# Kernel optimization log

Measured on AMD Instinct MI355X. Metric: run time of the kernel, lower is better.

Reference implementation:

```python
import jax, jax.numpy as jnp
import numpy as np

B, S, D = 4, 2048, 1024
H, HD = 16, 64  # num_heads, head_dim = qkv_features // num_heads


def setup_inputs() -> dict:
  key = jax.random.key(0)
  ks = jax.random.split(key, 11)
  s = 0.02
  return {
    'inputs_q': jax.random.normal(ks[0], (B, S, D), jnp.float32),
    'inputs_k': jax.random.normal(ks[1], (B, S, D), jnp.float32),
    'inputs_v': jax.random.normal(ks[2], (B, S, D), jnp.float32),
    # LinearGeneral kernels: [in_features, num_heads, head_dim]
    'Wq': jax.random.normal(ks[3], (D, H, HD), jnp.float32) * s,
    'bq': jnp.zeros((H, HD), jnp.float32),
    'Wk': jax.random.normal(ks[4], (D, H, HD), jnp.float32) * s,
    'bk': jnp.zeros((H, HD), jnp.float32),
    'Wv': jax.random.normal(ks[5], (D, H, HD), jnp.float32) * s,
    'bv': jnp.zeros((H, HD), jnp.float32),
    # output LinearGeneral kernel: [num_heads, head_dim, out_features]
    'Wo': jax.random.normal(ks[6], (H, HD, D), jnp.float32) * s,
    'bo': jnp.zeros((D,), jnp.float32),
  }


def reference(inputs_q, inputs_k, inputs_v, Wq, bq, Wk, bk, Wv, bv, Wo, bo):
  # q/k/v projections -> [B, S, H, HD]
  q = jnp.einsum('bsf,fhd->bshd', inputs_q, Wq) + bq
  k = jnp.einsum('bsf,fhd->bshd', inputs_k, Wk) + bk
  v = jnp.einsum('bsf,fhd->bshd', inputs_v, Wv) + bv
  # scaled dot-product attention (naive full softmax, as in the module)
  depth = q.shape[-1]
  q = q / jnp.sqrt(jnp.asarray(depth, q.dtype))
  attn = jnp.einsum('bqhd,bkhd->bhqk', q, k)  # [B, H, S, S]
  attn = jax.nn.softmax(attn, axis=-1)
  x = jnp.einsum('bhqk,bkhd->bqhd', attn, v)  # [B, S, H, HD]
  # output projection -> [B, S, D]
  out = jnp.einsum('bqhd,hdo->bqo', x, Wo) + bo
  return out
```

## Files before the change

kernel.cpp:

```cpp
#include <hip/hip_runtime.h>


typedef __attribute__((ext_vector_type(4))) float f32x4;
typedef __attribute__((ext_vector_type(8))) short short8;
typedef unsigned short u16;
typedef unsigned int u32;

__device__ __forceinline__ u16 f2bf(float f) {
  u32 u = __builtin_bit_cast(u32, f);
  u += 0x7fffu + ((u >> 16) & 1u);
  return (u16)(u >> 16);
}

__device__ __forceinline__ void gload16(const u16* g, u16* l) {
  __builtin_amdgcn_global_load_lds((const __attribute__((address_space(1))) void*)g,
                                   (__attribute__((address_space(3))) void*)l, 16, 0, 0);
}

__global__ __launch_bounds__(256) void cvt_f32_bf16(const float* __restrict__ in,
                                                    u16* __restrict__ out) {
  int i = blockIdx.x * 256 + threadIdx.x;
  float4 v = ((const float4*)in)[i];
  ushort4 o;
  o.x = f2bf(v.x); o.y = f2bf(v.y); o.z = f2bf(v.z); o.w = f2bf(v.w);
  ((ushort4*)out)[i] = o;
}

__global__ __launch_bounds__(256) void transpose_w(const float* __restrict__ src,
                                                   u16* __restrict__ dst) {
  __shared__ float t[64][65];
  const int bx = blockIdx.x * 64;
  const int by = blockIdx.y * 64;
  const int tid = threadIdx.x;
  const int c4 = (tid & 15) * 4, r = tid >> 4;
#pragma unroll
  for (int i = 0; i < 4; ++i) {
    int row = r + i * 16;
    float4 v = *(const float4*)&src[(size_t)(by + row) * 1024 + bx + c4];
    t[row][c4] = v.x; t[row][c4 + 1] = v.y; t[row][c4 + 2] = v.z; t[row][c4 + 3] = v.w;
  }
  __syncthreads();
#pragma unroll
  for (int i = 0; i < 4; ++i) {
    int nrow = r + i * 16;
    ushort4 o;
    o.x = f2bf(t[c4 + 0][nrow]); o.y = f2bf(t[c4 + 1][nrow]);
    o.z = f2bf(t[c4 + 2][nrow]); o.w = f2bf(t[c4 + 3][nrow]);
    *(ushort4*)&dst[(size_t)(bx + nrow) * 1024 + by + c4] = o;
  }
}

template <int EPI>
__global__ __launch_bounds__(256) void gemm_k1024(const u16* __restrict__ A,
                                                  const u16* __restrict__ Bt,
                                                  const float* __restrict__ bias,
                                                  void* __restrict__ outp) {
  __shared__ u16 lds[2 * 8192];
  u16* ldsA = lds;
  u16* ldsB = lds + 8192;
  const int tid = threadIdx.x, ln = tid & 63, wv = tid >> 6;
  const int wr = wv >> 1, wc = wv & 1;
  const int lq = ln & 15, g = ln >> 4;
  const int m0 = blockIdx.y * 128, n0 = blockIdx.x * 128;
  f32x4 acc[4][4] = {};

  for (int kt = 0; kt < 16; ++kt) {
    const int k0 = kt * 64;
#pragma unroll
    for (int c = 0; c < 4; ++c) {
      int chunk = c * 256 + wv * 64 + ln;
      int row = chunk >> 3, cc = chunk & 7;
      gload16(A + (size_t)(m0 + row) * 1024 + k0 + ((cc ^ (row & 7)) << 3),
              ldsA + (c * 256 + wv * 64) * 8);
    }
#pragma unroll
    for (int c = 0; c < 4; ++c) {
      int chunk = c * 256 + wv * 64 + ln;
      int row = chunk >> 3, cc = chunk & 7;
      gload16(Bt + (size_t)(n0 + row) * 1024 + k0 + ((cc ^ (row & 7)) << 3),
              ldsB + (c * 256 + wv * 64) * 8);
    }
    __syncthreads();
#pragma unroll
    for (int ks = 0; ks < 2; ++ks) {
      short8 af[4], bf[4];
#pragma unroll
      for (int m = 0; m < 4; ++m) {
        int rA = wr * 64 + m * 16 + lq;
        int cc = (ks * 4 + g) ^ (rA & 7);
        af[m] = *(const short8*)&ldsA[rA * 64 + cc * 8];
      }
#pragma unroll
      for (int n = 0; n < 4; ++n) {
        int rB = wc * 64 + n * 16 + lq;
        int cc = (ks * 4 + g) ^ (rB & 7);
        bf[n] = *(const short8*)&ldsB[rB * 64 + cc * 8];
      }
#pragma unroll
      for (int m = 0; m < 4; ++m)
#pragma unroll
        for (int n = 0; n < 4; ++n)
          acc[m][n] = __builtin_amdgcn_mfma_f32_16x16x32_bf16(af[m], bf[n], acc[m][n], 0, 0, 0);
    }
    __syncthreads();
  }

#pragma unroll
  for (int m = 0; m < 4; ++m) {
#pragma unroll
    for (int n = 0; n < 4; ++n) {
      const int row = m0 + wr * 64 + m * 16 + g * 4;
      const int col = n0 + wc * 64 + n * 16 + lq;
      const float bb = bias[col];
      if constexpr (EPI == 0 || EPI == 1) {
        u16* O = (u16*)outp;
        int b = row >> 11, s = row & 2047, h = col >> 6, d = col & 63;
        size_t base = ((size_t)(b * 16 + h) * 2048 + s) * 64 + d;
#pragma unroll
        for (int j = 0; j < 4; ++j) {
          float v = acc[m][n][j] + bb;
          if constexpr (EPI == 0) v *= 0.18033688f;
          O[base + (size_t)j * 64] = f2bf(v);
        }
      } else if constexpr (EPI == 2) {
        u16* O = (u16*)outp;
        int b = row >> 11, s = row & 2047, h = col >> 6, d = col & 63;
        ushort4 pk;
        pk.x = f2bf(acc[m][n][0] + bb); pk.y = f2bf(acc[m][n][1] + bb);
        pk.z = f2bf(acc[m][n][2] + bb); pk.w = f2bf(acc[m][n][3] + bb);
        *(ushort4*)&O[((size_t)(b * 16 + h) * 64 + d) * 2048 + s] = pk;
      } else {
        float* O = (float*)outp;
#pragma unroll
        for (int j = 0; j < 4; ++j) O[(size_t)(row + j) * 1024 + col] = acc[m][n][j] + bb;
      }
    }
  }
}

__global__ __launch_bounds__(256) void attn_kernel(const u16* __restrict__ Q,
                                                   const u16* __restrict__ K,
                                                   const u16* __restrict__ Vt,
                                                   u16* __restrict__ Xat) {
  __shared__ u16 lds[4096 + 4096 + 4 * 32 * 72];
  u16* ldsK = lds;
  u16* ldsV = lds + 4096;
  const int tid = threadIdx.x, ln = tid & 63, wv = tid >> 6;
  const int lq = ln & 15, g = ln >> 4;
  const int bh = blockIdx.y;
  const int q0 = blockIdx.x * 128 + wv * 32;
  u16* myP = lds + 8192 + wv * 32 * 72;

  const u16* Qb = Q + ((size_t)bh * 2048 + q0) * 64;
  const u16* Kb = K + (size_t)bh * 2048 * 64;
  const u16* Vb = Vt + (size_t)bh * 64 * 2048;

  short8 qf[2][2];
#pragma unroll
  for (int qb = 0; qb < 2; ++qb)
#pragma unroll
    for (int ks = 0; ks < 2; ++ks)
      qf[qb][ks] = *(const short8*)&Qb[(size_t)(qb * 16 + lq) * 64 + ks * 32 + g * 8];

  f32x4 accO[2][4] = {};
  float lsum[2] = {0.f, 0.f};

  for (int kv = 0; kv < 32; ++kv) {
    const int s0 = kv * 64;
#pragma unroll
    for (int c = 0; c < 2; ++c) {
      int chunk = c * 256 + wv * 64 + ln;
      int row = chunk >> 3, cc = chunk & 7;
      gload16(Kb + (size_t)(s0 + row) * 64 + ((cc ^ (row & 7)) << 3),
              ldsK + (c * 256 + wv * 64) * 8);
    }
#pragma unroll
    for (int c = 0; c < 2; ++c) {
      int chunk = c * 256 + wv * 64 + ln;
      int row = chunk >> 3, cc = chunk & 7;
      gload16(Vb + (size_t)row * 2048 + s0 + ((cc ^ (row & 7)) << 3),
              ldsV + (c * 256 + wv * 64) * 8);
    }
    __syncthreads();

    f32x4 accS[4][2] = {};
#pragma unroll
    for (int ks = 0; ks < 2; ++ks) {
      short8 kf[4];
#pragma unroll
      for (int m = 0; m < 4; ++m) {
        int r = m * 16 + lq;
        int cc = (ks * 4 + g) ^ (r & 7);
        kf[m] = *(const short8*)&ldsK[r * 64 + cc * 8];
      }
#pragma unroll
      for (int m = 0; m < 4; ++m)
#pragma unroll
        for (int qb = 0; qb < 2; ++qb)
          accS[m][qb] = __builtin_amdgcn_mfma_f32_16x16x32_bf16(kf[m], qf[qb][ks], accS[m][qb], 0, 0, 0);
    }

#pragma unroll
    for (int qb = 0; qb < 2; ++qb) {
      float p[16];
#pragma unroll
      for (int m = 0; m < 4; ++m)
#pragma unroll
        for (int j = 0; j < 4; ++j) {
          float v = exp2f(accS[m][qb][j]);
          p[m * 4 + j] = v;
          lsum[qb] += v;
        }
#pragma unroll
      for (int m = 0; m < 4; ++m) {
        u32 w0, w1;
        asm("v_cvt_pk_bf16_f32 %0, %1, %2" : "=v"(w0) : "v"(p[m * 4 + 0]), "v"(p[m * 4 + 1]));
        asm("v_cvt_pk_bf16_f32 %0, %1, %2" : "=v"(w1) : "v"(p[m * 4 + 2]), "v"(p[m * 4 + 3]));
        uint2 w; w.x = w0; w.y = w1;
        *(uint2*)&myP[(qb * 16 + lq) * 72 + m * 16 + g * 4] = w;
      }
    }

#pragma unroll
    for (int ks = 0; ks < 2; ++ks) {
      short8 pf[2];
#pragma unroll
      for (int qb = 0; qb < 2; ++qb)
        pf[qb] = *(const short8*)&myP[(qb * 16 + lq) * 72 + ks * 32 + g * 8];
#pragma unroll
      for (int n = 0; n < 4; ++n) {
        int r = n * 16 + lq;
        int cc = (ks * 4 + g) ^ (r & 7);
        short8 vf = *(const short8*)&ldsV[r * 64 + cc * 8];
#pragma unroll
        for (int qb = 0; qb < 2; ++qb)
          accO[qb][n] = __builtin_amdgcn_mfma_f32_16x16x32_bf16(pf[qb], vf, accO[qb][n], 0, 0, 0);
      }
    }
    __syncthreads();
  }

  const int b = bh >> 4, h = bh & 15;
#pragma unroll
  for (int qb = 0; qb < 2; ++qb) {
    float t = lsum[qb];
    t += __shfl_xor(t, 16);
    t += __shfl_xor(t, 32);
    float inv = 1.0f / t;
    float inv_row[4];
#pragma unroll
    for (int j = 0; j < 4; ++j) inv_row[j] = __shfl(inv, g * 4 + j);
#pragma unroll
    for (int n = 0; n < 4; ++n)
#pragma unroll
      for (int j = 0; j < 4; ++j) {
        int s = q0 + qb * 16 + g * 4 + j;
        Xat[((size_t)b * 2048 + s) * 1024 + h * 64 + n * 16 + lq] = f2bf(accO[qb][n][j] * inv_row[j]);
      }
  }
}

extern "C" void kernel_launch(void* const* d_in, const int* in_sizes, int n_in,
                              void* d_out, int out_size, void* d_ws, size_t ws_size,
                              hipStream_t stream) {
  const float* xq = (const float*)d_in[0];
  const float* xk = (const float*)d_in[1];
  const float* xv = (const float*)d_in[2];
  const float* Wq = (const float*)d_in[3];
  const float* bq = (const float*)d_in[4];
  const float* Wk = (const float*)d_in[5];
  const float* bk = (const float*)d_in[6];
  const float* Wv = (const float*)d_in[7];
  const float* bv = (const float*)d_in[8];
  const float* Wo = (const float*)d_in[9];
  const float* bo = (const float*)d_in[10];

  char* ws = (char*)d_ws;
  u16* Xqb = (u16*)(ws + 0);
  u16* Xkb = (u16*)(ws + 16777216);
  u16* Xvb = (u16*)(ws + 33554432);
  u16* Wtq = (u16*)(ws + 50331648);
  u16* Wtk = (u16*)(ws + 52428800);
  u16* Wtv = (u16*)(ws + 54525952);
  u16* Wot = (u16*)(ws + 56623104);
  u16* Qb  = (u16*)(ws + 58720256);
  u16* Kb  = (u16*)(ws + 75497472);
  u16* Vtb = (u16*)(ws + 92274688);
  u16* Xat = Xqb;

  cvt_f32_bf16<<<8192, 256, 0, stream>>>(xq, Xqb);
  cvt_f32_bf16<<<8192, 256, 0, stream>>>(xk, Xkb);
  cvt_f32_bf16<<<8192, 256, 0, stream>>>(xv, Xvb);

  transpose_w<<<dim3(16, 16), 256, 0, stream>>>(Wq, Wtq);
  transpose_w<<<dim3(16, 16), 256, 0, stream>>>(Wk, Wtk);
  transpose_w<<<dim3(16, 16), 256, 0, stream>>>(Wv, Wtv);
  transpose_w<<<dim3(16, 16), 256, 0, stream>>>(Wo, Wot);

  gemm_k1024<0><<<dim3(8, 64), 256, 0, stream>>>(Xqb, Wtq, bq, Qb);
  gemm_k1024<1><<<dim3(8, 64), 256, 0, stream>>>(Xkb, Wtk, bk, Kb);
  gemm_k1024<2><<<dim3(8, 64), 256, 0, stream>>>(Xvb, Wtv, bv, Vtb);

  attn_kernel<<<dim3(16, 64), 256, 0, stream>>>(Qb, Kb, Vtb, Xat);

  gemm_k1024<3><<<dim3(8, 64), 256, 0, stream>>>(Xat, Wot, bo, d_out);
}
```

Measured before the change: 394.5 us.

## Double-buffer attention K/V loads, compute row sums via MFMA, batch prep kernels

The attention kernel now double-buffers K/V tiles in LDS, issuing the next tile's async global-to-LDS loads before computing the current one, so memory latency overlaps with the MFMA work. Softmax row sums are now accumulated with an extra MFMA against a ones vector instead of scalar adds and cross-lane shuffles. The three f32-to-bf16 conversions and four weight transposes are each merged into a single launch. The changes cost twice the K/V LDS, which may reduce occupancy, plus extra barriers, and the row sums are now taken from bf16-rounded probabilities.

```diff
diff --git a/kernel.cpp b/kernel.cpp
--- a/kernel.cpp
+++ b/kernel.cpp
@@ -17,8 +17,14 @@
                                    (__attribute__((address_space(3))) void*)l, 16, 0, 0);
 }
 
-__global__ __launch_bounds__(256) void cvt_f32_bf16(const float* __restrict__ in,
-                                                    u16* __restrict__ out) {
+__global__ __launch_bounds__(256) void cvt_f32_bf16_3(const float* __restrict__ a,
+                                                      const float* __restrict__ b,
+                                                      const float* __restrict__ c,
+                                                      u16* __restrict__ oa,
+                                                      u16* __restrict__ ob,
+                                                      u16* __restrict__ oc) {
+  const float* in = blockIdx.y == 0 ? a : (blockIdx.y == 1 ? b : c);
+  u16* out = blockIdx.y == 0 ? oa : (blockIdx.y == 1 ? ob : oc);
   int i = blockIdx.x * 256 + threadIdx.x;
   float4 v = ((const float4*)in)[i];
   ushort4 o;
@@ -26,8 +32,16 @@
   ((ushort4*)out)[i] = o;
 }
 
-__global__ __launch_bounds__(256) void transpose_w(const float* __restrict__ src,
-                                                   u16* __restrict__ dst) {
+__global__ __launch_bounds__(256) void transpose_w4(const float* __restrict__ s0,
+                                                    const float* __restrict__ s1,
+                                                    const float* __restrict__ s2,
+                                                    const float* __restrict__ s3,
+                                                    u16* __restrict__ d0,
+                                                    u16* __restrict__ d1,
+                                                    u16* __restrict__ d2,
+                                                    u16* __restrict__ d3) {
+  const float* src = blockIdx.z == 0 ? s0 : (blockIdx.z == 1 ? s1 : (blockIdx.z == 2 ? s2 : s3));
+  u16* dst = blockIdx.z == 0 ? d0 : (blockIdx.z == 1 ? d1 : (blockIdx.z == 2 ? d2 : d3));
   __shared__ float t[64][65];
   const int bx = blockIdx.x * 64;
   const int by = blockIdx.y * 64;
@@ -142,14 +156,16 @@
                                                    const u16* __restrict__ K,
                                                    const u16* __restrict__ Vt,
                                                    u16* __restrict__ Xat) {
-  __shared__ u16 lds[4096 + 4096 + 4 * 32 * 72];
-  u16* ldsK = lds;
-  u16* ldsV = lds + 4096;
+  __shared__ u16 lds[4 * 4096 + 4 * 32 * 72];
+  u16* ldsK0 = lds;
+  u16* ldsK1 = lds + 4096;
+  u16* ldsV0 = lds + 8192;
+  u16* ldsV1 = lds + 12288;
   const int tid = threadIdx.x, ln = tid & 63, wv = tid >> 6;
   const int lq = ln & 15, g = ln >> 4;
   const int bh = blockIdx.y;
   const int q0 = blockIdx.x * 128 + wv * 32;
-  u16* myP = lds + 8192 + wv * 32 * 72;
+  u16* myP = lds + 16384 + wv * 32 * 72;
 
   const u16* Qb = Q + ((size_t)bh * 2048 + q0) * 64;
   const u16* Kb = K + (size_t)bh * 2048 * 64;
@@ -162,27 +178,31 @@
     for (int ks = 0; ks < 2; ++ks)
       qf[qb][ks] = *(const short8*)&Qb[(size_t)(qb * 16 + lq) * 64 + ks * 32 + g * 8];
 
+  short8 ones;
+#pragma unroll
+  for (int i = 0; i < 8; ++i) ones[i] = (short)0x3F80;
+
   f32x4 accO[2][4] = {};
-  float lsum[2] = {0.f, 0.f};
-
-  for (int kv = 0; kv < 32; ++kv) {
-    const int s0 = kv * 64;
+  f32x4 accL[2] = {};
+
+  auto stage = [&](int s0, u16* dK, u16* dV) {
 #pragma unroll
     for (int c = 0; c < 2; ++c) {
       int chunk = c * 256 + wv * 64 + ln;
       int row = chunk >> 3, cc = chunk & 7;
       gload16(Kb + (size_t)(s0 + row) * 64 + ((cc ^ (row & 7)) << 3),
-              ldsK + (c * 256 + wv * 64) * 8);
+              dK + (c * 256 + wv * 64) * 8);
     }
 #pragma unroll
     for (int c = 0; c < 2; ++c) {
       int chunk = c * 256 + wv * 64 + ln;
       int row = chunk >> 3, cc = chunk & 7;
       gload16(Vb + (size_t)row * 2048 + s0 + ((cc ^ (row & 7)) << 3),
-              ldsV + (c * 256 + wv * 64) * 8);
-    }
-    __syncthreads();
-
+              dV + (c * 256 + wv * 64) * 8);
+    }
+  };
+
+  auto compute = [&](const u16* cK, const u16* cV) {
     f32x4 accS[4][2] = {};
 #pragma unroll
     for (int ks = 0; ks < 2; ++ks) {
@@ -191,7 +211,7 @@
       for (int m = 0; m < 4; ++m) {
         int r = m * 16 + lq;
         int cc = (ks * 4 + g) ^ (r & 7);
-        kf[m] = *(const short8*)&ldsK[r * 64 + cc * 8];
+        kf[m] = *(const short8*)&cK[r * 64 + cc * 8];
       }
 #pragma unroll
       for (int m = 0; m < 4; ++m)
@@ -199,18 +219,13 @@
         for (int qb = 0; qb < 2; ++qb)
           accS[m][qb] = __builtin_amdgcn_mfma_f32_16x16x32_bf16(kf[m], qf[qb][ks], accS[m][qb], 0, 0, 0);
     }
-
 #pragma unroll
     for (int qb = 0; qb < 2; ++qb) {
       float p[16];
 #pragma unroll
       for (int m = 0; m < 4; ++m)
 #pragma unroll
-        for (int j = 0; j < 4; ++j) {
-          float v = exp2f(accS[m][qb][j]);
-          p[m * 4 + j] = v;
-          lsum[qb] += v;
-        }
+        for (int j = 0; j < 4; ++j) p[m * 4 + j] = exp2f(accS[m][qb][j]);
 #pragma unroll
       for (int m = 0; m < 4; ++m) {
         u32 w0, w1;
@@ -220,36 +235,57 @@
         *(uint2*)&myP[(qb * 16 + lq) * 72 + m * 16 + g * 4] = w;
       }
     }
-
 #pragma unroll
     for (int ks = 0; ks < 2; ++ks) {
       short8 pf[2];
 #pragma unroll
       for (int qb = 0; qb < 2; ++qb)
         pf[qb] = *(const short8*)&myP[(qb * 16 + lq) * 72 + ks * 32 + g * 8];
+#pragma unroll
+      for (int qb = 0; qb < 2; ++qb)
+        accL[qb] = __builtin_amdgcn_mfma_f32_16x16x32_bf16(pf[qb], ones, accL[qb], 0, 0, 0);
 #pragma unroll
       for (int n = 0; n < 4; ++n) {
         int r = n * 16 + lq;
         int cc = (ks * 4 + g) ^ (r & 7);
-        short8 vf = *(const short8*)&ldsV[r * 64 + cc * 8];
+        short8 vf = *(const short8*)&cV[r * 64 + cc * 8];
 #pragma unroll
         for (int qb = 0; qb < 2; ++qb)
           accO[qb][n] = __builtin_amdgcn_mfma_f32_16x16x32_bf16(pf[qb], vf, accO[qb][n], 0, 0, 0);
       }
     }
-    __syncthreads();
+  };
+
+  stage(0, ldsK0, ldsV0);
+
+  for (int t = 0; t < 16; ++t) {
+    const int kv0 = 2 * t;
+    stage((kv0 + 1) * 64, ldsK1, ldsV1);
+    asm volatile("s_waitcnt vmcnt(4)" ::: "memory");
+    __builtin_amdgcn_s_barrier();
+    __builtin_amdgcn_sched_barrier(0);
+    compute(ldsK0, ldsV0);
+    __builtin_amdgcn_s_barrier();
+    __builtin_amdgcn_sched_barrier(0);
+    if (t < 15) {
+      stage((kv0 + 2) * 64, ldsK0, ldsV0);
+      asm volatile("s_waitcnt vmcnt(4)" ::: "memory");
+    } else {
+      asm volatile("s_waitcnt vmcnt(0)" ::: "memory");
+    }
+    __builtin_amdgcn_s_barrier();
+    __builtin_amdgcn_sched_barrier(0);
+    compute(ldsK1, ldsV1);
+    __builtin_amdgcn_s_barrier();
+    __builtin_amdgcn_sched_barrier(0);
   }
 
   const int b = bh >> 4, h = bh & 15;
 #pragma unroll
   for (int qb = 0; qb < 2; ++qb) {
-    float t = lsum[qb];
-    t += __shfl_xor(t, 16);
-    t += __shfl_xor(t, 32);
-    float inv = 1.0f / t;
     float inv_row[4];
 #pragma unroll
-    for (int j = 0; j < 4; ++j) inv_row[j] = __shfl(inv, g * 4 + j);
+    for (int j = 0; j < 4; ++j) inv_row[j] = 1.0f / accL[qb][j];
 #pragma unroll
     for (int n = 0; n < 4; ++n)
 #pragma unroll
@@ -288,14 +324,8 @@
   u16* Vtb = (u16*)(ws + 92274688);
   u16* Xat = Xqb;
 
-  cvt_f32_bf16<<<8192, 256, 0, stream>>>(xq, Xqb);
-  cvt_f32_bf16<<<8192, 256, 0, stream>>>(xk, Xkb);
-  cvt_f32_bf16<<<8192, 256, 0, stream>>>(xv, Xvb);
-
-  transpose_w<<<dim3(16, 16), 256, 0, stream>>>(Wq, Wtq);
-  transpose_w<<<dim3(16, 16), 256, 0, stream>>>(Wk, Wtk);
-  transpose_w<<<dim3(16, 16), 256, 0, stream>>>(Wv, Wtv);
-  transpose_w<<<dim3(16, 16), 256, 0, stream>>>(Wo, Wot);
+  cvt_f32_bf16_3<<<dim3(8192, 3), 256, 0, stream>>>(xq, xk, xv, Xqb, Xkb, Xvb);
+  transpose_w4<<<dim3(16, 16, 4), 256, 0, stream>>>(Wq, Wk, Wv, Wo, Wtq, Wtk, Wtv, Wot);
 
   gemm_k1024<0><<<dim3(8, 64), 256, 0, stream>>>(Xqb, Wtq, bq, Qb);
   gemm_k1024<1><<<dim3(8, 64), 256, 0, stream>>>(Xkb, Wtk, bk, Kb);
```

Result: faster. 378.6 us (-4.0%).
